# Optimization experiments

Hardware: AMD Instinct MI355X
Metric: run time of the kernel (lower is better)

## Reference

```python
import jax, jax.numpy as jnp
import numpy as np

B, L, D = 2, 2048, 2560
H, KV, HD = 8, 4, 256
FF = 10240
WINDOW = 1024
ROPE_BASE = 10000.0
EPS = 1e-6


def rmsnorm(x, scale=None):
    x32 = x.astype(jnp.float32)
    var = jnp.mean(jnp.square(x32), axis=-1, keepdims=True)
    xn = x32 * jax.lax.rsqrt(var + EPS)
    return xn if scale is None else xn * scale.astype(jnp.float32)


def apply_rope(x, positions, base):
    # full RoPE (rope_fraction=1.0): rotate pairs (i, i+head_dim//2)
    hd = x.shape[-1]
    half = hd // 2
    timescale = base ** (2.0 * jnp.arange(half, dtype=jnp.float32) / hd)
    ang = positions[:, :, None].astype(jnp.float32) / timescale  # [B,L,half]
    sin = jnp.sin(ang)[:, :, None, :]  # [B,L,1,half]
    cos = jnp.cos(ang)[:, :, None, :]
    x1, x2 = x[..., :half], x[..., half:]
    return jnp.concatenate([x1 * cos - x2 * sin, x2 * cos + x1 * sin], axis=-1)


def setup_inputs() -> dict:
    key = jax.random.key(0)
    ks = jax.random.split(key, 16)
    s = lambda fan_in: 1.0 / np.sqrt(fan_in)
    return {
        "x": jax.random.normal(ks[0], (B, L, D), jnp.float32),
        "positions": jnp.broadcast_to(jnp.arange(L, dtype=jnp.int32), (B, L)),
        "wq": jax.random.normal(ks[1], (D, H * HD), jnp.float32) * s(D),
        "wk": jax.random.normal(ks[2], (D, KV * HD), jnp.float32) * s(D),
        "wv": jax.random.normal(ks[3], (D, KV * HD), jnp.float32) * s(D),
        "wo": jax.random.normal(ks[4], (H * HD, D), jnp.float32) * s(H * HD),
        "q_scale": jnp.ones((HD,), jnp.float32),
        "k_scale": jnp.ones((HD,), jnp.float32),
        "pre_attn_scale": jnp.ones((D,), jnp.float32),
        "post_attn_scale": jnp.ones((D,), jnp.float32),
        "pre_ffw_scale": jnp.ones((D,), jnp.float32),
        "post_ffw_scale": jnp.ones((D,), jnp.float32),
        "w_gate": jax.random.normal(ks[5], (D, FF), jnp.float32) * s(D),
        "w_up": jax.random.normal(ks[6], (D, FF), jnp.float32) * s(D),
        "w_down": jax.random.normal(ks[7], (FF, D), jnp.float32) * s(FF),
    }


def reference(x, positions, wq, wk, wv, wo, q_scale, k_scale,
              pre_attn_scale, post_attn_scale, pre_ffw_scale, post_ffw_scale,
              w_gate, w_up, w_down):
    # --- attention sub-block ---
    h = rmsnorm(x, pre_attn_scale)
    q = (h @ wq).reshape(B, L, H, HD)
    k = (h @ wk).reshape(B, L, KV, HD)
    v = (h @ wv).reshape(B, L, KV, HD)
    q = apply_rope(rmsnorm(q, q_scale), positions, ROPE_BASE)
    k = apply_rope(rmsnorm(k, k_scale), positions, ROPE_BASE)
    v = rmsnorm(v)  # RMSNormNoScale on V
    rep = H // KV
    k = jnp.repeat(k, rep, axis=2)  # [B,L,H,HD]
    v = jnp.repeat(v, rep, axis=2)
    scores = jnp.einsum("bqhd,bkhd->bhqk", q, k)  # NOTE: no 1/sqrt(d) scaling, faithful to source
    i = jnp.arange(L)[:, None]
    j = jnp.arange(L)[None, :]
    mask = (j <= i) & (j > i - WINDOW)  # causal & sliding window
    scores = jnp.where(mask[None, None, :, :], scores, -10000.0)
    probs = jax.nn.softmax(scores.astype(jnp.float32), axis=-1)
    attn = jnp.einsum("bhqk,bkhd->bqhd", probs, v).reshape(B, L, H * HD)
    attn = attn @ wo
    x = x + rmsnorm(attn, post_attn_scale)
    # --- feedforward sub-block (GeGLU) ---
    h = rmsnorm(x, pre_ffw_scale)
    hidden = jax.nn.gelu(h @ w_gate, approximate=False) * (h @ w_up)
    ffw = hidden @ w_down
    x = x + rmsnorm(ffw, post_ffw_scale)
    return x
```

## Files before the change

kernel.cpp:

```cpp
#include <hip/hip_runtime.h>
#include <math.h>

#define DEV __device__ __forceinline__

typedef _Float16 f16;
typedef _Float16 f16x8 __attribute__((ext_vector_type(8)));
typedef _Float16 f16x4 __attribute__((ext_vector_type(4)));
typedef float f32x4 __attribute__((ext_vector_type(4)));

DEV void gload_lds16(const void* g, void* l) {
  __builtin_amdgcn_global_load_lds(
      (const __attribute__((address_space(1))) void*)g,
      (__attribute__((address_space(3))) void*)l, 16, 0, 0);
}

__global__ __launch_bounds__(256) void transpose_w64(
    const float* __restrict__ src, f16* __restrict__ dst, int R, int C) {
  __shared__ float tile[64][65];
  const int r0 = blockIdx.y * 64, c0 = blockIdx.x * 64;
  const int tid = threadIdx.x;
  const int rr = tid >> 4;
  const int rc = (tid & 15) * 4;
#pragma unroll
  for (int p = 0; p < 4; ++p) {
    int r = p * 16 + rr;
    float4 v = *(const float4*)(src + (size_t)(r0 + r) * C + c0 + rc);
    tile[r][rc] = v.x; tile[r][rc + 1] = v.y;
    tile[r][rc + 2] = v.z; tile[r][rc + 3] = v.w;
  }
  __syncthreads();
  const int wc = tid >> 3;
  const int wk = (tid & 7) * 8;
#pragma unroll
  for (int p = 0; p < 2; ++p) {
    int c = p * 32 + wc;
    f16x8 o;
#pragma unroll
    for (int i = 0; i < 8; ++i) o[i] = (f16)tile[wk + i][c];
    *(f16x8*)(dst + (size_t)(c0 + c) * R + r0 + wk) = o;
  }
}

__global__ void rope_table_k(float* __restrict__ tab) {
  int idx = blockIdx.x * 256 + threadIdx.x;
  int pos = idx >> 7, j = idx & 127;
  float ts = powf(10000.0f, (float)j * (1.0f / 128.0f));
  float ang = (float)pos / ts;
  tab[pos * 256 + j] = sinf(ang);
  tab[pos * 256 + 128 + j] = cosf(ang);
}

__global__ __launch_bounds__(256) void rmsnorm_f32_f16(
    const float* __restrict__ in, const float* __restrict__ scale,
    f16* __restrict__ out) {
  constexpr int D = 2560, N4 = D / 4;
  const int m = blockIdx.x, tid = threadIdx.x;
  const float* row = in + (size_t)m * D;
  float vals[12];
  float ss = 0.f;
#pragma unroll
  for (int it = 0; it < 3; ++it) {
    int c4 = tid + it * 256;
    if (c4 < N4) {
      float4 v = *(const float4*)(row + c4 * 4);
      vals[it * 4 + 0] = v.x; vals[it * 4 + 1] = v.y;
      vals[it * 4 + 2] = v.z; vals[it * 4 + 3] = v.w;
      ss += v.x * v.x + v.y * v.y + v.z * v.z + v.w * v.w;
    }
  }
#pragma unroll
  for (int off = 32; off; off >>= 1) ss += __shfl_xor(ss, off, 64);
  __shared__ float red[4];
  if ((tid & 63) == 0) red[tid >> 6] = ss;
  __syncthreads();
  float rs = rsqrtf((red[0] + red[1] + red[2] + red[3]) * (1.0f / D) + 1e-6f);
#pragma unroll
  for (int it = 0; it < 3; ++it) {
    int c4 = tid + it * 256;
    if (c4 < N4) {
      float4 sc = *(const float4*)(scale + c4 * 4);
      f16x4 o;
      o[0] = (f16)(vals[it * 4 + 0] * rs * sc.x);
      o[1] = (f16)(vals[it * 4 + 1] * rs * sc.y);
      o[2] = (f16)(vals[it * 4 + 2] * rs * sc.z);
      o[3] = (f16)(vals[it * 4 + 3] * rs * sc.w);
      *(f16x4*)(out + (size_t)m * D + c4 * 4) = o;
    }
  }
}

__global__ __launch_bounds__(256) void residual_rmsnorm3(
    const float* __restrict__ x, const f16* __restrict__ y0,
    const f16* __restrict__ y1, const f16* __restrict__ y2,
    const float* __restrict__ scale, float* __restrict__ out,
    const float* __restrict__ scale2, f16* __restrict__ h) {
  constexpr int D = 2560, N4 = D / 4;
  const int m = blockIdx.x, tid = threadIdx.x;
  const size_t base = (size_t)m * D;
  __shared__ float red[4];
  float yv[12];
  float ss = 0.f;
#pragma unroll
  for (int it = 0; it < 3; ++it) {
    int c4 = tid + it * 256;
    if (c4 < N4) {
      f16x4 u = *(const f16x4*)(y0 + base + c4 * 4);
      float a = (float)u[0], b = (float)u[1], c = (float)u[2], d = (float)u[3];
      if (y1) {
        f16x4 v = *(const f16x4*)(y1 + base + c4 * 4);
        f16x4 w2 = *(const f16x4*)(y2 + base + c4 * 4);
        a += (float)v[0] + (float)w2[0]; b += (float)v[1] + (float)w2[1];
        c += (float)v[2] + (float)w2[2]; d += (float)v[3] + (float)w2[3];
      }
      yv[it * 4 + 0] = a; yv[it * 4 + 1] = b; yv[it * 4 + 2] = c; yv[it * 4 + 3] = d;
      ss += a * a + b * b + c * c + d * d;
    }
  }
#pragma unroll
  for (int off = 32; off; off >>= 1) ss += __shfl_xor(ss, off, 64);
  if ((tid & 63) == 0) red[tid >> 6] = ss;
  __syncthreads();
  float rs = rsqrtf((red[0] + red[1] + red[2] + red[3]) * (1.0f / D) + 1e-6f);
  float ss2 = 0.f;
#pragma unroll
  for (int it = 0; it < 3; ++it) {
    int c4 = tid + it * 256;
    if (c4 < N4) {
      float4 xv = *(const float4*)(x + base + c4 * 4);
      float4 sc = *(const float4*)(scale + c4 * 4);
      float4 o;
      o.x = xv.x + yv[it * 4 + 0] * rs * sc.x;
      o.y = xv.y + yv[it * 4 + 1] * rs * sc.y;
      o.z = xv.z + yv[it * 4 + 2] * rs * sc.z;
      o.w = xv.w + yv[it * 4 + 3] * rs * sc.w;
      *(float4*)(out + base + c4 * 4) = o;
      yv[it * 4 + 0] = o.x; yv[it * 4 + 1] = o.y;
      yv[it * 4 + 2] = o.z; yv[it * 4 + 3] = o.w;
      ss2 += o.x * o.x + o.y * o.y + o.z * o.z + o.w * o.w;
    }
  }
  if (h) {
#pragma unroll
    for (int off = 32; off; off >>= 1) ss2 += __shfl_xor(ss2, off, 64);
    __syncthreads();
    if ((tid & 63) == 0) red[tid >> 6] = ss2;
    __syncthreads();
    float rs2 = rsqrtf((red[0] + red[1] + red[2] + red[3]) * (1.0f / D) + 1e-6f);
#pragma unroll
    for (int it = 0; it < 3; ++it) {
      int c4 = tid + it * 256;
      if (c4 < N4) {
        float4 sc = *(const float4*)(scale2 + c4 * 4);
        f16x4 o;
        o[0] = (f16)(yv[it * 4 + 0] * rs2 * sc.x);
        o[1] = (f16)(yv[it * 4 + 1] * rs2 * sc.y);
        o[2] = (f16)(yv[it * 4 + 2] * rs2 * sc.z);
        o[3] = (f16)(yv[it * 4 + 3] * rs2 * sc.w);
        *(f16x4*)(h + base + c4 * 4) = o;
      }
    }
  }
}

__global__ __launch_bounds__(256) void norm_rope_k(
    const f16* __restrict__ qkv, const int* __restrict__ positions,
    const float* __restrict__ q_scale, const float* __restrict__ k_scale,
    const float* __restrict__ tab,
    f16* __restrict__ q_g, f16* __restrict__ k_g, f16* __restrict__ v_n) {
  const int m = blockIdx.x;
  const int tid = threadIdx.x, w = tid >> 6, l = tid & 63;
  const int pos = positions[m];
  const float* srow = tab + (size_t)pos * 256;
  const int c0 = l * 4;
  for (int vi = w; vi < 16; vi += 4) {
    f16x4 u = *(const f16x4*)(qkv + (size_t)m * 4096 + vi * 256 + c0);
    float x0 = (float)u[0], x1 = (float)u[1], x2 = (float)u[2], x3 = (float)u[3];
    float ss = x0 * x0 + x1 * x1 + x2 * x2 + x3 * x3;
#pragma unroll
    for (int off = 32; off; off >>= 1) ss += __shfl_xor(ss, off, 64);
    float rs = rsqrtf(ss * (1.0f / 256.0f) + 1e-6f);
    if (vi < 12) {
      const float* sc = (vi < 8) ? q_scale : k_scale;
      float4 s4 = *(const float4*)(sc + c0);
      float n0 = x0 * rs * s4.x, n1 = x1 * rs * s4.y;
      float n2 = x2 * rs * s4.z, n3 = x3 * rs * s4.w;
      float p0 = __shfl_xor(n0, 32, 64), p1 = __shfl_xor(n1, 32, 64);
      float p2 = __shfl_xor(n2, 32, 64), p3 = __shfl_xor(n3, 32, 64);
      int j0 = c0 & 127;
      float4 sn = *(const float4*)(srow + j0);
      float4 cs = *(const float4*)(srow + 128 + j0);
      float sgn = (l < 32) ? -1.0f : 1.0f;
      f16x4 o;
      o[0] = (f16)(n0 * cs.x + sgn * p0 * sn.x);
      o[1] = (f16)(n1 * cs.y + sgn * p1 * sn.y);
      o[2] = (f16)(n2 * cs.z + sgn * p2 * sn.z);
      o[3] = (f16)(n3 * cs.w + sgn * p3 * sn.w);
      if (vi < 8) *(f16x4*)(q_g + (size_t)m * 2048 + vi * 256 + c0) = o;
      else        *(f16x4*)(k_g + (size_t)m * 1024 + (vi - 8) * 256 + c0) = o;
    } else {
      f16x4 o;
      o[0] = (f16)(x0 * rs); o[1] = (f16)(x1 * rs);
      o[2] = (f16)(x2 * rs); o[3] = (f16)(x3 * rs);
      *(f16x4*)(v_n + (size_t)m * 1024 + (vi - 12) * 256 + c0) = o;
    }
  }
}

__global__ void transpose_v_k(const f16* __restrict__ v_n, f16* __restrict__ vt) {
  __shared__ f16 tile[32][33];
  int bkv = blockIdx.z;
  int b = bkv >> 2, kv = bkv & 3;
  int t0 = blockIdx.x * 32, d0 = blockIdx.y * 32;
  int tx = threadIdx.x, ty = threadIdx.y;
#pragma unroll
  for (int j = 0; j < 32; j += 8)
    tile[ty + j][tx] =
        v_n[(size_t)(b * 2048 + t0 + ty + j) * 1024 + kv * 256 + d0 + tx];
  __syncthreads();
#pragma unroll
  for (int j = 0; j < 32; j += 8)
    vt[((size_t)bkv * 256 + d0 + ty + j) * 2048 + t0 + tx] = tile[tx][ty + j];
}

template <int EPI>
__global__ __launch_bounds__(512, 2) void gemm256(
    const f16* __restrict__ A, const f16* __restrict__ BT,
    f16* __restrict__ C, f16* __restrict__ aux, int M, int N, int K,
    int kt0, int ktn) {
  extern __shared__ __align__(16) f16 lds[];
  const int tid = threadIdx.x;
  const int w = tid >> 6, l = tid & 63;
  const int l15 = l & 15, lk = l >> 4;
  const int wm = w >> 2, wn = w & 3;

  const int orig = blockIdx.y * gridDim.x + blockIdx.x;
  const int bm = orig & 15;
  int bn, sK = 0;
  if constexpr (EPI == 4) {
    const int nper = (((int)(gridDim.x * gridDim.y)) >> 4) / 3;
    const int q = orig >> 4;
    bn = q % nper; sK = q / nper;
  } else {
    bn = orig >> 4;
  }
  int kt0v, ktnv;
  if constexpr (EPI == 4) {
    const int qt = ktn / 3, r = ktn % 3;
    ktnv = qt + (sK < r ? 1 : 0);
    kt0v = kt0 + sK * qt + (sK < r ? sK : r);
  } else {
    kt0v = kt0; ktnv = ktn;
  }
  const int NT = ktnv;

  const int srow = tid >> 2;
  const int sg = (tid & 3) ^ ((srow >> 1) & 3);
  const f16* src0 = A + (size_t)(bm * 256 + srow) * K + sg * 8 + kt0v * 32;
  const f16* src1 = src0 + (size_t)128 * K;
  const f16* src2;
  const f16* src3;
  if constexpr (EPI == 3) {
    src2 = BT + (size_t)(bn * 128 + srow) * K + sg * 8 + kt0v * 32;
    src3 = aux + (size_t)(bn * 128 + srow) * K + sg * 8 + kt0v * 32;
  } else {
    src2 = BT + (size_t)(bn * 256 + srow) * K + sg * 8 + kt0v * 32;
    src3 = src2 + (size_t)128 * K;
  }

  auto stage = [&](int buf, int kt) {
    f16* base = lds + buf * 16384 + tid * 8;
    const int kb = kt * 32;
    gload_lds16(src0 + kb, base);
    gload_lds16(src1 + kb, base + 4096);
    gload_lds16(src2 + kb, base + 8192);
    gload_lds16(src3 + kb, base + 12288);
  };

  const int fcol = (lk ^ ((l15 >> 1) & 3)) << 3;
  const int aoff = wm * 4096 + l15 * 32 + fcol;
  int boff;
  if constexpr (EPI != 3) {
    boff = (2 + (wn >> 1)) * 4096 + ((wn & 1) * 64 + l15) * 32 + fcol;
  } else {
    boff = 8192 + (wn * 32 + l15) * 32 + fcol;
  }

  f32x4 acc[8][4] = {};

  stage(0, 0);
  if (NT > 1) {
    stage(1, 1);
    asm volatile("s_waitcnt vmcnt(4)" ::: "memory");
  } else {
    asm volatile("s_waitcnt vmcnt(0)" ::: "memory");
  }
  __builtin_amdgcn_s_barrier();
  asm volatile("" ::: "memory");

  int buf = 0;
  for (int t = 0; t < NT; ++t) {
    const int bb = buf * 16384;
    f16x8 a[8], b[4];
#pragma unroll
    for (int i = 0; i < 8; ++i) a[i] = *(const f16x8*)(lds + bb + aoff + i * 512);
    if constexpr (EPI == 3) {
      b[0] = *(const f16x8*)(lds + bb + boff);
      b[1] = *(const f16x8*)(lds + bb + boff + 512);
      b[2] = *(const f16x8*)(lds + bb + boff + 4096);
      b[3] = *(const f16x8*)(lds + bb + boff + 4096 + 512);
    } else {
#pragma unroll
      for (int i = 0; i < 4; ++i) b[i] = *(const f16x8*)(lds + bb + boff + i * 512);
    }
    if (t + 2 < NT) {
      int nb = buf + 2; if (nb >= 3) nb -= 3;
      stage(nb, t + 2);
    }
    __builtin_amdgcn_s_setprio(1);
#pragma unroll
    for (int mi = 0; mi < 8; ++mi)
#pragma unroll
      for (int ni = 0; ni < 4; ++ni)
        acc[mi][ni] = __builtin_amdgcn_mfma_f32_16x16x32_f16(a[mi], b[ni], acc[mi][ni], 0, 0, 0);
    __builtin_amdgcn_s_setprio(0);
    if (t + 1 < NT) {
      if (t + 2 < NT) asm volatile("s_waitcnt vmcnt(4)" ::: "memory");
      else            asm volatile("s_waitcnt vmcnt(0)" ::: "memory");
      __builtin_amdgcn_s_barrier();
      asm volatile("" ::: "memory");
    }
    ++buf; if (buf >= 3) buf = 0;
  }

  if constexpr (EPI == 3) {
#pragma unroll
    for (int mi = 0; mi < 8; ++mi)
#pragma unroll
      for (int ni = 0; ni < 2; ++ni)
#pragma unroll
        for (int i = 0; i < 4; ++i) {
          int row = bm * 256 + wm * 128 + mi * 16 + lk * 4 + i;
          int col = bn * 128 + wn * 32 + ni * 16 + l15;
          float g = acc[mi][ni][i];
          g = 0.5f * g * (1.0f + erff(g * 0.70710678118654752f));
          C[(size_t)row * N + col] = (f16)(g * acc[mi][ni + 2][i]);
        }
  } else {
    f16* Co = C;
    if constexpr (EPI == 4) {
      if (sK) Co = aux + (size_t)(sK - 1) * ((size_t)M * N);
    }
#pragma unroll
    for (int mi = 0; mi < 8; ++mi) {
#pragma unroll
      for (int ni = 0; ni < 4; ++ni) {
#pragma unroll
        for (int i = 0; i < 4; ++i) {
          int row = bm * 256 + wm * 128 + mi * 16 + lk * 4 + i;
          int col = bn * 256 + wn * 64 + ni * 16 + l15;
          size_t idx = (size_t)row * N + col;
          float v = acc[mi][ni][i];
          if constexpr (EPI == 1) {
            v = 0.5f * v * (1.0f + erff(v * 0.70710678118654752f));
          } else if constexpr (EPI == 2) {
            v *= (float)aux[idx];
          }
          Co[idx] = (f16)v;
        }
      }
    }
  }
}

__global__ __launch_bounds__(256) void flash_attn_k(
    const f16* __restrict__ q_g, const f16* __restrict__ k_g,
    const f16* __restrict__ vt, f16* __restrict__ ctx) {
  constexpr int KP = 264, VP = 40, PP = 40;
  __shared__ f16 Ks[32 * KP];
  __shared__ f16 Vs[256 * VP];
  __shared__ f16 Ps[4][16 * PP];
  const int qt = blockIdx.x, h = blockIdx.y, b = blockIdx.z;
  const int tid = threadIdx.x, w = tid >> 6, l = tid & 63;
  const int l15 = l & 15, lk = l >> 4;
  const int kv = h >> 1;

  f16x8 aq[8];
  const int qrow = qt * 64 + w * 16 + l15;
  const f16* qp = q_g + (size_t)(b * 2048 + qrow) * 2048 + h * 256 + lk * 8;
#pragma unroll
  for (int kc = 0; kc < 8; ++kc) aq[kc] = *(const f16x8*)(qp + kc * 32);

  f32x4 o[16] = {};
  float mrow[4] = {-1e30f, -1e30f, -1e30f, -1e30f};
  float lrow[4] = {0.f, 0.f, 0.f, 0.f};

  int kt_lo = 2 * qt - 32; if (kt_lo < 0) kt_lo = 0;
  const int kt_hi = 2 * qt + 1;
  const int iqb = qt * 64 + w * 16 + lk * 4;

  for (int kt = kt_lo; kt <= kt_hi; ++kt) {
    __syncthreads();
#pragma unroll
    for (int it = 0; it < 4; ++it) {
      int ch = tid + it * 256;
      int jl = ch >> 5, kcc = (ch & 31) * 8;
      *(f16x8*)&Ks[jl * KP + kcc] = *(const f16x8*)(
          k_g + (size_t)(b * 2048 + kt * 32 + jl) * 1024 + kv * 256 + kcc);
      int d = ch >> 2, tc = (ch & 3) * 8;
      *(f16x8*)&Vs[d * VP + tc] = *(const f16x8*)(
          vt + ((size_t)(b * 4 + kv) * 256 + d) * 2048 + kt * 32 + tc);
    }
    __syncthreads();
    f32x4 s[2] = {};
#pragma unroll
    for (int ct = 0; ct < 2; ++ct)
#pragma unroll
      for (int kc = 0; kc < 8; ++kc) {
        f16x8 bk = *(const f16x8*)&Ks[(ct * 16 + l15) * KP + kc * 32 + lk * 8];
        s[ct] = __builtin_amdgcn_mfma_f32_16x16x32_f16(aq[kc], bk, s[ct], 0, 0, 0);
      }
    float pm[4] = {-1e30f, -1e30f, -1e30f, -1e30f};
#pragma unroll
    for (int ct = 0; ct < 2; ++ct)
#pragma unroll
      for (int i = 0; i < 4; ++i) {
        int iq = iqb + i;
        int j = kt * 32 + ct * 16 + l15;
        bool valid = (j <= iq) && (j > iq - 1024);
        float sv = valid ? s[ct][i] : -1e30f;
        s[ct][i] = sv;
        pm[i] = fmaxf(pm[i], sv);
      }
#pragma unroll
    for (int i = 0; i < 4; ++i)
#pragma unroll
      for (int off = 1; off < 16; off <<= 1)
        pm[i] = fmaxf(pm[i], __shfl_xor(pm[i], off, 64));
    float corr[4], rsum[4];
#pragma unroll
    for (int i = 0; i < 4; ++i) {
      float mn = fmaxf(mrow[i], pm[i]);
      corr[i] = __expf(mrow[i] - mn);
      mrow[i] = mn;
      rsum[i] = 0.f;
    }
#pragma unroll
    for (int ct = 0; ct < 2; ++ct)
#pragma unroll
      for (int i = 0; i < 4; ++i) {
        float p = (s[ct][i] > -1e29f) ? __expf(s[ct][i] - mrow[i]) : 0.f;
        s[ct][i] = p;
        rsum[i] += p;
      }
#pragma unroll
    for (int i = 0; i < 4; ++i) {
#pragma unroll
      for (int off = 1; off < 16; off <<= 1) rsum[i] += __shfl_xor(rsum[i], off, 64);
      lrow[i] = lrow[i] * corr[i] + rsum[i];
    }
#pragma unroll
    for (int dt = 0; dt < 16; ++dt)
#pragma unroll
      for (int i = 0; i < 4; ++i) o[dt][i] *= corr[i];
#pragma unroll
    for (int ct = 0; ct < 2; ++ct)
#pragma unroll
      for (int i = 0; i < 4; ++i)
        Ps[w][(lk * 4 + i) * PP + ct * 16 + l15] = (f16)s[ct][i];
    __syncthreads();
    f16x8 pa = *(const f16x8*)&Ps[w][l15 * PP + lk * 8];
#pragma unroll
    for (int dt = 0; dt < 16; ++dt) {
      f16x8 bv = *(const f16x8*)&Vs[(dt * 16 + l15) * VP + lk * 8];
      o[dt] = __builtin_amdgcn_mfma_f32_16x16x32_f16(pa, bv, o[dt], 0, 0, 0);
    }
  }
  float inv[4];
#pragma unroll
  for (int i = 0; i < 4; ++i) inv[i] = 1.0f / lrow[i];
  f16* op = ctx + (size_t)(b * 2048 + qt * 64 + w * 16 + lk * 4) * 2048 + h * 256 + l15;
#pragma unroll
  for (int dt = 0; dt < 16; ++dt)
#pragma unroll
    for (int i = 0; i < 4; ++i)
      op[(size_t)i * 2048 + dt * 16] = (f16)(o[dt][i] * inv[i]);
}

extern "C" void kernel_launch(void* const* d_in, const int* in_sizes, int n_in,
                              void* d_out, int out_size, void* d_ws, size_t ws_size,
                              hipStream_t stream) {
  const float* x = (const float*)d_in[0];
  const int* positions = (const int*)d_in[1];
  const float* wq = (const float*)d_in[2];
  const float* wk = (const float*)d_in[3];
  const float* wv = (const float*)d_in[4];
  const float* wo = (const float*)d_in[5];
  const float* q_scale = (const float*)d_in[6];
  const float* k_scale = (const float*)d_in[7];
  const float* pre_attn = (const float*)d_in[8];
  const float* post_attn = (const float*)d_in[9];
  const float* pre_ffw = (const float*)d_in[10];
  const float* post_ffw = (const float*)d_in[11];
  const float* w_gate = (const float*)d_in[12];
  const float* w_up = (const float*)d_in[13];
  const float* w_down = (const float*)d_in[14];
  float* out = (float*)d_out;

  static bool s_attr = []() {
    hipFuncSetAttribute(reinterpret_cast<const void*>(&gemm256<0>),
                        hipFuncAttributeMaxDynamicSharedMemorySize, 98304);
    hipFuncSetAttribute(reinterpret_cast<const void*>(&gemm256<1>),
                        hipFuncAttributeMaxDynamicSharedMemorySize, 98304);
    hipFuncSetAttribute(reinterpret_cast<const void*>(&gemm256<2>),
                        hipFuncAttributeMaxDynamicSharedMemorySize, 98304);
    hipFuncSetAttribute(reinterpret_cast<const void*>(&gemm256<3>),
                        hipFuncAttributeMaxDynamicSharedMemorySize, 98304);
    hipFuncSetAttribute(reinterpret_cast<const void*>(&gemm256<4>),
                        hipFuncAttributeMaxDynamicSharedMemorySize, 98304);
    return true;
  }();
  (void)s_attr;

  const size_t WT_BIG   = (size_t)20480 * 2560 * 2;
  const size_t WT_SMALL = (size_t)10240 * 2560 * 2;
  const size_t TAB_B = (size_t)2048 * 256 * 4;
  const size_t H_B   = (size_t)4096 * 2560 * 2;
  const size_t ACT_B = (size_t)92280832;
  auto aln = [](size_t v) { return (v + 255) & ~(size_t)255; };
  const bool big = ws_size >= aln(WT_BIG) + aln(TAB_B) + aln(H_B) + aln(ACT_B);

  char* ws = (char*)d_ws;
  size_t off = 0;
  auto alloc = [&](size_t bytes) {
    char* p = ws + off;
    off += (bytes + 255) & ~(size_t)255;
    return p;
  };
  f16* wT    = (f16*)alloc(big ? WT_BIG : WT_SMALL);
  float* tab = (float*)alloc(TAB_B);
  f16* h     = (f16*)alloc(H_B);
  char* act  = alloc(ACT_B);
  f16* qkv    = (f16*)(act);
  f16* q_g    = (f16*)(act + (size_t)33554432);
  f16* k_g    = (f16*)(act + (size_t)33554432 + 16777216);
  f16* v_n    = (f16*)(act + (size_t)33554432 + 16777216 + 8388608);
  f16* vtb    = (f16*)(act + (size_t)33554432 + 16777216 + 2 * 8388608);
  f16* ctx    = (f16*)(act + (size_t)33554432 + 16777216 + 3 * 8388608);
  f16* attn_o = (f16*)(act);
  f16* gbuf = (f16*)(act);
  f16* ffw  = h;
  f16* wuT  = wT + (size_t)10240 * 2560;
  f16* ap1  = wuT;
  f16* fp1  = wT;
  (void)in_sizes; (void)n_in; (void)out_size;

  rope_table_k<<<1024, 256, 0, stream>>>(tab);

  rmsnorm_f32_f16<<<4096, 256, 0, stream>>>(x, pre_attn, h);
  transpose_w64<<<dim3(2048 / 64, 2560 / 64), 256, 0, stream>>>(wq, wT, 2560, 2048);
  transpose_w64<<<dim3(1024 / 64, 2560 / 64), 256, 0, stream>>>(wk, wT + (size_t)2048 * 2560, 2560, 1024);
  transpose_w64<<<dim3(1024 / 64, 2560 / 64), 256, 0, stream>>>(wv, wT + (size_t)3072 * 2560, 2560, 1024);
  gemm256<0><<<dim3(16, 16), 512, 98304, stream>>>(h, wT, qkv, nullptr, 4096, 4096, 2560, 0, 80);
  norm_rope_k<<<4096, 256, 0, stream>>>(qkv, positions, q_scale, k_scale, tab, q_g, k_g, v_n);
  transpose_v_k<<<dim3(2048 / 32, 256 / 32, 8), dim3(32, 8), 0, stream>>>(v_n, vtb);
  flash_attn_k<<<dim3(32, 8, 2), 256, 0, stream>>>(q_g, k_g, vtb, ctx);
  transpose_w64<<<dim3(2560 / 64, 2048 / 64), 256, 0, stream>>>(wo, wT, 2048, 2560);
  if (big) {
    gemm256<4><<<dim3(30, 16), 512, 98304, stream>>>(ctx, wT, attn_o, ap1, 4096, 2560, 2048, 0, 64);
    residual_rmsnorm3<<<4096, 256, 0, stream>>>(x, attn_o, ap1, ap1 + (size_t)4096 * 2560,
                                                post_attn, out, pre_ffw, h);
  } else {
    gemm256<0><<<dim3(10, 16), 512, 98304, stream>>>(ctx, wT, attn_o, nullptr, 4096, 2560, 2048, 0, 64);
    residual_rmsnorm3<<<4096, 256, 0, stream>>>(x, attn_o, nullptr, nullptr,
                                                post_attn, out, pre_ffw, h);
  }

  if (big) {
    transpose_w64<<<dim3(10240 / 64, 2560 / 64), 256, 0, stream>>>(w_gate, wT, 2560, 10240);
    transpose_w64<<<dim3(10240 / 64, 2560 / 64), 256, 0, stream>>>(w_up, wuT, 2560, 10240);
    gemm256<3><<<dim3(80, 16), 512, 98304, stream>>>(h, wT, gbuf, wuT, 4096, 10240, 2560, 0, 80);
    transpose_w64<<<dim3(2560 / 64, 10240 / 64), 256, 0, stream>>>(w_down, wuT, 10240, 2560);
    gemm256<4><<<dim3(30, 16), 512, 98304, stream>>>(gbuf, wuT, ffw, fp1, 4096, 2560, 10240, 0, 320);
    residual_rmsnorm3<<<4096, 256, 0, stream>>>(out, ffw, fp1, fp1 + (size_t)4096 * 2560,
                                                post_ffw, out, nullptr, nullptr);
  } else {
    transpose_w64<<<dim3(10240 / 64, 2560 / 64), 256, 0, stream>>>(w_gate, wT, 2560, 10240);
    gemm256<1><<<dim3(40, 16), 512, 98304, stream>>>(h, wT, gbuf, nullptr, 4096, 10240, 2560, 0, 80);
    transpose_w64<<<dim3(10240 / 64, 2560 / 64), 256, 0, stream>>>(w_up, wT, 2560, 10240);
    gemm256<2><<<dim3(40, 16), 512, 98304, stream>>>(h, wT, gbuf, gbuf, 4096, 10240, 2560, 0, 80);
    transpose_w64<<<dim3(2560 / 64, 10240 / 64), 256, 0, stream>>>(w_down, wT, 10240, 2560);
    gemm256<0><<<dim3(10, 16), 512, 98304, stream>>>(gbuf, wT, ffw, nullptr, 4096, 2560, 10240, 0, 320);
    residual_rmsnorm3<<<4096, 256, 0, stream>>>(out, ffw, nullptr, nullptr,
                                                post_ffw, out, nullptr, nullptr);
  }
}
```

Measured before the change: 1.092 ms.

## Deepen GEMM pipeline to four LDS stages with register double-buffered fragments

The GEMM main loop moves from a three-buffer LDS ring to four buffers, keeping global-to-LDS loads three tiles ahead. Operand fragments are now double-buffered in registers: the next tile's A/B fragments load from LDS while the second half of the current tile's MFMAs runs, and each tile is split into two MFMA halves so the second A fragment loads overlap the first half's math. The goal is to hide LDS and global latency behind MFMA work. The cost is raising dynamic shared memory from 96 KB to 128 KB per block and using more registers, which may limit occupancy.

Result: no change. 1.100 ms (+0.8%).

```diff
diff --git a/kernel.cpp b/kernel.cpp
--- a/kernel.cpp
+++ b/kernel.cpp
@@ -286,51 +286,84 @@
   }
 
   f32x4 acc[8][4] = {};
+  f16x8 aP[4], bP[4], aQ[4], bQ[4];
 
   stage(0, 0);
-  if (NT > 1) {
-    stage(1, 1);
-    asm volatile("s_waitcnt vmcnt(4)" ::: "memory");
-  } else {
-    asm volatile("s_waitcnt vmcnt(0)" ::: "memory");
-  }
+  if (NT > 1) stage(1, 1);
+  if (NT > 2) stage(2, 2);
+  if (NT > 2) asm volatile("s_waitcnt vmcnt(4)" ::: "memory");
+  else        asm volatile("s_waitcnt vmcnt(0)" ::: "memory");
   __builtin_amdgcn_s_barrier();
   asm volatile("" ::: "memory");
-
-  int buf = 0;
-  for (int t = 0; t < NT; ++t) {
-    const int bb = buf * 16384;
-    f16x8 a[8], b[4];
-#pragma unroll
-    for (int i = 0; i < 8; ++i) a[i] = *(const f16x8*)(lds + bb + aoff + i * 512);
-    if constexpr (EPI == 3) {
-      b[0] = *(const f16x8*)(lds + bb + boff);
-      b[1] = *(const f16x8*)(lds + bb + boff + 512);
-      b[2] = *(const f16x8*)(lds + bb + boff + 4096);
-      b[3] = *(const f16x8*)(lds + bb + boff + 4096 + 512);
-    } else {
-#pragma unroll
-      for (int i = 0; i < 4; ++i) b[i] = *(const f16x8*)(lds + bb + boff + i * 512);
-    }
-    if (t + 2 < NT) {
-      int nb = buf + 2; if (nb >= 3) nb -= 3;
-      stage(nb, t + 2);
-    }
-    __builtin_amdgcn_s_setprio(1);
-#pragma unroll
-    for (int mi = 0; mi < 8; ++mi)
-#pragma unroll
-      for (int ni = 0; ni < 4; ++ni)
-        acc[mi][ni] = __builtin_amdgcn_mfma_f32_16x16x32_f16(a[mi], b[ni], acc[mi][ni], 0, 0, 0);
-    __builtin_amdgcn_s_setprio(0);
-    if (t + 1 < NT) {
-      if (t + 2 < NT) asm volatile("s_waitcnt vmcnt(4)" ::: "memory");
-      else            asm volatile("s_waitcnt vmcnt(0)" ::: "memory");
-      __builtin_amdgcn_s_barrier();
-      asm volatile("" ::: "memory");
-    }
-    ++buf; if (buf >= 3) buf = 0;
-  }
+#pragma unroll
+  for (int i = 0; i < 4; ++i) aP[i] = *(const f16x8*)(lds + aoff + i * 512);
+  if constexpr (EPI == 3) {
+    bP[0] = *(const f16x8*)(lds + boff);
+    bP[1] = *(const f16x8*)(lds + boff + 512);
+    bP[2] = *(const f16x8*)(lds + boff + 4096);
+    bP[3] = *(const f16x8*)(lds + boff + 4096 + 512);
+  } else {
+#pragma unroll
+    for (int i = 0; i < 4; ++i) bP[i] = *(const f16x8*)(lds + boff + i * 512);
+  }
+  asm volatile("s_waitcnt lgkmcnt(0)" ::: "memory");
+  __builtin_amdgcn_s_barrier();
+  asm volatile("" ::: "memory");
+
+#define GEMM_TILE(CA, CB, NA, NB, T)                                           \
+  {                                                                            \
+    const int bb_ = ((T) & 3) * 16384;                                         \
+    if ((T) + 3 < NT) stage(((T) + 3) & 3, (T) + 3);                           \
+    f16x8 a2_[4];                                                              \
+    _Pragma("unroll")                                                          \
+    for (int i_ = 0; i_ < 4; ++i_)                                             \
+      a2_[i_] = *(const f16x8*)(lds + bb_ + aoff + (4 + i_) * 512);            \
+    __builtin_amdgcn_s_setprio(1);                                             \
+    _Pragma("unroll")                                                          \
+    for (int mi_ = 0; mi_ < 4; ++mi_)                                          \
+      _Pragma("unroll")                                                        \
+      for (int ni_ = 0; ni_ < 4; ++ni_)                                        \
+        acc[mi_][ni_] = __builtin_amdgcn_mfma_f32_16x16x32_f16(                \
+            CA[mi_], CB[ni_], acc[mi_][ni_], 0, 0, 0);                         \
+    __builtin_amdgcn_s_setprio(0);                                             \
+    if ((T) + 1 < NT) {                                                        \
+      const int nb_ = (((T) + 1) & 3) * 16384;                                 \
+      _Pragma("unroll")                                                        \
+      for (int i_ = 0; i_ < 4; ++i_)                                           \
+        NA[i_] = *(const f16x8*)(lds + nb_ + aoff + i_ * 512);                 \
+      if constexpr (EPI == 3) {                                                \
+        NB[0] = *(const f16x8*)(lds + nb_ + boff);                             \
+        NB[1] = *(const f16x8*)(lds + nb_ + boff + 512);                       \
+        NB[2] = *(const f16x8*)(lds + nb_ + boff + 4096);                      \
+        NB[3] = *(const f16x8*)(lds + nb_ + boff + 4096 + 512);                \
+      } else {                                                                 \
+        _Pragma("unroll")                                                      \
+        for (int i_ = 0; i_ < 4; ++i_)                                         \
+          NB[i_] = *(const f16x8*)(lds + nb_ + boff + i_ * 512);               \
+      }                                                                        \
+    }                                                                          \
+    __builtin_amdgcn_s_setprio(1);                                             \
+    _Pragma("unroll")                                                          \
+    for (int mi_ = 0; mi_ < 4; ++mi_)                                          \
+      _Pragma("unroll")                                                        \
+      for (int ni_ = 0; ni_ < 4; ++ni_)                                        \
+        acc[4 + mi_][ni_] = __builtin_amdgcn_mfma_f32_16x16x32_f16(            \
+            a2_[mi_], CB[ni_], acc[4 + mi_][ni_], 0, 0, 0);                    \
+    __builtin_amdgcn_s_setprio(0);                                             \
+    asm volatile("s_waitcnt lgkmcnt(0)" ::: "memory");                         \
+    if ((T) + 3 < NT) asm volatile("s_waitcnt vmcnt(4)" ::: "memory");         \
+    else              asm volatile("s_waitcnt vmcnt(0)" ::: "memory");         \
+    __builtin_amdgcn_s_barrier();                                              \
+    asm volatile("" ::: "memory");                                             \
+  }
+
+  int t = 0;
+  for (; t + 1 < NT; t += 2) {
+    GEMM_TILE(aP, bP, aQ, bQ, t);
+    GEMM_TILE(aQ, bQ, aP, bP, t + 1);
+  }
+  if (t < NT) GEMM_TILE(aP, bP, aQ, bQ, t);
+#undef GEMM_TILE
 
   if constexpr (EPI == 3) {
 #pragma unroll
@@ -508,15 +541,15 @@
 
   static bool s_attr = []() {
     hipFuncSetAttribute(reinterpret_cast<const void*>(&gemm256<0>),
-                        hipFuncAttributeMaxDynamicSharedMemorySize, 98304);
+                        hipFuncAttributeMaxDynamicSharedMemorySize, 131072);
     hipFuncSetAttribute(reinterpret_cast<const void*>(&gemm256<1>),
-                        hipFuncAttributeMaxDynamicSharedMemorySize, 98304);
+                        hipFuncAttributeMaxDynamicSharedMemorySize, 131072);
     hipFuncSetAttribute(reinterpret_cast<const void*>(&gemm256<2>),
-                        hipFuncAttributeMaxDynamicSharedMemorySize, 98304);
+                        hipFuncAttributeMaxDynamicSharedMemorySize, 131072);
     hipFuncSetAttribute(reinterpret_cast<const void*>(&gemm256<3>),
-                        hipFuncAttributeMaxDynamicSharedMemorySize, 98304);
+                        hipFuncAttributeMaxDynamicSharedMemorySize, 131072);
     hipFuncSetAttribute(reinterpret_cast<const void*>(&gemm256<4>),
-                        hipFuncAttributeMaxDynamicSharedMemorySize, 98304);
+                        hipFuncAttributeMaxDynamicSharedMemorySize, 131072);
     return true;
   }();
   (void)s_attr;
@@ -560,17 +593,17 @@
   transpose_w64<<<dim3(2048 / 64, 2560 / 64), 256, 0, stream>>>(wq, wT, 2560, 2048);
   transpose_w64<<<dim3(1024 / 64, 2560 / 64), 256, 0, stream>>>(wk, wT + (size_t)2048 * 2560, 2560, 1024);
   transpose_w64<<<dim3(1024 / 64, 2560 / 64), 256, 0, stream>>>(wv, wT + (size_t)3072 * 2560, 2560, 1024);
-  gemm256<0><<<dim3(16, 16), 512, 98304, stream>>>(h, wT, qkv, nullptr, 4096, 4096, 2560, 0, 80);
+  gemm256<0><<<dim3(16, 16), 512, 131072, stream>>>(h, wT, qkv, nullptr, 4096, 4096, 2560, 0, 80);
   norm_rope_k<<<4096, 256, 0, stream>>>(qkv, positions, q_scale, k_scale, tab, q_g, k_g, v_n);
   transpose_v_k<<<dim3(2048 / 32, 256 / 32, 8), dim3(32, 8), 0, stream>>>(v_n, vtb);
   flash_attn_k<<<dim3(32, 8, 2), 256, 0, stream>>>(q_g, k_g, vtb, ctx);
   transpose_w64<<<dim3(2560 / 64, 2048 / 64), 256, 0, stream>>>(wo, wT, 2048, 2560);
   if (big) {
-    gemm256<4><<<dim3(30, 16), 512, 98304, stream>>>(ctx, wT, attn_o, ap1, 4096, 2560, 2048, 0, 64);
+    gemm256<4><<<dim3(30, 16), 512, 131072, stream>>>(ctx, wT, attn_o, ap1, 4096, 2560, 2048, 0, 64);
     residual_rmsnorm3<<<4096, 256, 0, stream>>>(x, attn_o, ap1, ap1 + (size_t)4096 * 2560,
                                                 post_attn, out, pre_ffw, h);
   } else {
-    gemm256<0><<<dim3(10, 16), 512, 98304, stream>>>(ctx, wT, attn_o, nullptr, 4096, 2560, 2048, 0, 64);
+    gemm256<0><<<dim3(10, 16), 512, 131072, stream>>>(ctx, wT, attn_o, nullptr, 4096, 2560, 2048, 0, 64);
     residual_rmsnorm3<<<4096, 256, 0, stream>>>(x, attn_o, nullptr, nullptr,
                                                 post_attn, out, pre_ffw, h);
   }
@@ -578,18 +611,18 @@
   if (big) {
     transpose_w64<<<dim3(10240 / 64, 2560 / 64), 256, 0, stream>>>(w_gate, wT, 2560, 10240);
     transpose_w64<<<dim3(10240 / 64, 2560 / 64), 256, 0, stream>>>(w_up, wuT, 2560, 10240);
-    gemm256<3><<<dim3(80, 16), 512, 98304, stream>>>(h, wT, gbuf, wuT, 4096, 10240, 2560, 0, 80);
+    gemm256<3><<<dim3(80, 16), 512, 131072, stream>>>(h, wT, gbuf, wuT, 4096, 10240, 2560, 0, 80);
     transpose_w64<<<dim3(2560 / 64, 10240 / 64), 256, 0, stream>>>(w_down, wuT, 10240, 2560);
-    gemm256<4><<<dim3(30, 16), 512, 98304, stream>>>(gbuf, wuT, ffw, fp1, 4096, 2560, 10240, 0, 320);
+    gemm256<4><<<dim3(30, 16), 512, 131072, stream>>>(gbuf, wuT, ffw, fp1, 4096, 2560, 10240, 0, 320);
     residual_rmsnorm3<<<4096, 256, 0, stream>>>(out, ffw, fp1, fp1 + (size_t)4096 * 2560,
                                                 post_ffw, out, nullptr, nullptr);
   } else {
     transpose_w64<<<dim3(10240 / 64, 2560 / 64), 256, 0, stream>>>(w_gate, wT, 2560, 10240);
-    gemm256<1><<<dim3(40, 16), 512, 98304, stream>>>(h, wT, gbuf, nullptr, 4096, 10240, 2560, 0, 80);
+    gemm256<1><<<dim3(40, 16), 512, 131072, stream>>>(h, wT, gbuf, nullptr, 4096, 10240, 2560, 0, 80);
     transpose_w64<<<dim3(10240 / 64, 2560 / 64), 256, 0, stream>>>(w_up, wT, 2560, 10240);
-    gemm256<2><<<dim3(40, 16), 512, 98304, stream>>>(h, wT, gbuf, gbuf, 4096, 10240, 2560, 0, 80);
+    gemm256<2><<<dim3(40, 16), 512, 131072, stream>>>(h, wT, gbuf, gbuf, 4096, 10240, 2560, 0, 80);
     transpose_w64<<<dim3(2560 / 64, 10240 / 64), 256, 0, stream>>>(w_down, wT, 10240, 2560);
-    gemm256<0><<<dim3(10, 16), 512, 98304, stream>>>(gbuf, wT, ffw, nullptr, 4096, 2560, 10240, 0, 320);
+    gemm256<0><<<dim3(10, 16), 512, 131072, stream>>>(gbuf, wT, ffw, nullptr, 4096, 2560, 10240, 0, 320);
     residual_rmsnorm3<<<4096, 256, 0, stream>>>(out, ffw, nullptr, nullptr,
                                                 post_ffw, out, nullptr, nullptr);
   }
```
